# Performance work log

Hardware: AMD Instinct MI355X
Metric: run time of the kernel (lower is better)

## Reference

```python
import jax, jax.numpy as jnp
from jax import lax
import numpy as np

WS = 8      # window_size
SS = 4      # shift_size
NH = 8      # num_heads
DIM = 192
HID = int(DIM * 2.66)  # 510


def _rel_pos_index(ws):
    coords = np.stack(np.meshgrid(np.arange(ws), np.arange(ws), indexing='ij'))
    flat = coords.reshape(2, -1)
    rel = (flat[:, :, None] - flat[:, None, :]).transpose(1, 2, 0)
    rel[..., 0] += ws - 1
    rel[..., 1] += ws - 1
    rel[..., 0] *= 2 * ws - 1
    return rel.sum(-1)  # (ws*ws, ws*ws) int


def _attn_mask(Hp, Wp, ws, ss):
    img = np.zeros((Hp, Wp), dtype=np.float32)
    slices = (slice(0, -ws), slice(-ws, -ss), slice(-ss, None))
    cnt = 0
    for h in slices:
        for w in slices:
            img[h, w] = cnt
            cnt += 1
    mw = img.reshape(Hp // ws, ws, Wp // ws, ws).transpose(0, 2, 1, 3).reshape(-1, ws * ws)
    am = mw[:, None, :] - mw[:, :, None]
    return np.where(am != 0, -100.0, 0.0).astype(np.float32)  # (nW, N, N)


def _ln(t, w, b):
    mu = t.mean(-1, keepdims=True)
    var = t.var(-1, keepdims=True)
    return (t - mu) / jnp.sqrt(var + 1e-5) * w + b


def setup_inputs() -> dict:
    key = jax.random.key(0)
    ks = jax.random.split(key, 12)
    s = 0.05
    return {
        'x': jax.random.normal(ks[0], (2, DIM, 256, 256), jnp.float32),
        'norm1_w': jnp.ones((DIM,), jnp.float32),
        'norm1_b': jnp.zeros((DIM,), jnp.float32),
        'qkv_w': jax.random.normal(ks[1], (3 * DIM, DIM), jnp.float32) * s,
        'rpb_table': jax.random.normal(ks[2], ((2 * WS - 1) * (2 * WS - 1), NH), jnp.float32) * 0.02,
        'proj_w': jax.random.normal(ks[3], (DIM, DIM), jnp.float32) * s,
        'proj_b': jnp.zeros((DIM,), jnp.float32),
        'norm2_w': jnp.ones((DIM,), jnp.float32),
        'norm2_b': jnp.zeros((DIM,), jnp.float32),
        'pin_w': jax.random.normal(ks[4], (2 * HID, DIM), jnp.float32) * s,
        'dw_w': jax.random.normal(ks[5], (2 * HID, 1, 3, 3), jnp.float32) * s,
        'pout_w': jax.random.normal(ks[6], (DIM, HID), jnp.float32) * s,
    }


def reference(x, norm1_w, norm1_b, qkv_w, rpb_table, proj_w, proj_b,
              norm2_w, norm2_b, pin_w, dw_w, pout_w):
    B, C, H, W = x.shape
    hd = C // NH
    scale = hd ** -0.5

    # ---- norm1 (channel-last layernorm) ----
    xc = jnp.transpose(x, (0, 2, 3, 1))  # BHWC
    xn = _ln(xc, norm1_w, norm1_b)

    # ---- pad to window multiple ----
    pad_b = (WS - H % WS) % WS
    pad_r = (WS - W % WS) % WS
    xn = jnp.pad(xn, ((0, 0), (0, pad_b), (0, pad_r), (0, 0)))
    Hp, Wp = H + pad_b, W + pad_r

    # ---- cyclic shift ----
    sx = jnp.roll(xn, (-SS, -SS), axis=(1, 2))

    # ---- window partition ----
    nH, nW = Hp // WS, Wp // WS
    N = WS * WS
    xw = sx.reshape(B, nH, WS, nW, WS, C).transpose(0, 1, 3, 2, 4, 5)
    xw = xw.reshape(B * nH * nW, N, C)

    # ---- window attention ----
    qkv = (xw @ qkv_w.T).reshape(-1, N, 3, NH, hd).transpose(2, 0, 3, 1, 4)
    q, k, v = qkv[0] * scale, qkv[1], qkv[2]  # (B_, NH, N, hd)
    attn = jnp.einsum('bhnd,bhmd->bhnm', q, k)

    idx = _rel_pos_index(WS)
    bias = rpb_table[idx.reshape(-1)].reshape(N, N, NH).transpose(2, 0, 1)
    attn = attn + bias[None]

    mask = jnp.asarray(_attn_mask(Hp, Wp, WS, SS))  # (nWtot, N, N)
    nWtot = nH * nW
    attn = attn.reshape(B, nWtot, NH, N, N) + mask[None, :, None]
    attn = jax.nn.softmax(attn.reshape(-1, NH, N, N), axis=-1)

    out = jnp.einsum('bhnm,bhmd->bhnd', attn, v)
    out = out.transpose(0, 2, 1, 3).reshape(-1, N, C)
    out = out @ proj_w.T + proj_b

    # ---- window reverse + unshift + crop ----
    out = out.reshape(B, nH, nW, WS, WS, C).transpose(0, 1, 3, 2, 4, 5)
    out = out.reshape(B, Hp, Wp, C)
    out = jnp.roll(out, (SS, SS), axis=(1, 2))[:, :H, :W]
    x = x + jnp.transpose(out, (0, 3, 1, 2))

    # ---- FFN: 1x1 in -> depthwise 3x3 -> gated gelu -> 1x1 out ----
    y = _ln(jnp.transpose(x, (0, 2, 3, 1)), norm2_w, norm2_b)
    y = jnp.transpose(y, (0, 3, 1, 2))
    y = jnp.einsum('bchw,oc->bohw', y, pin_w)
    y = lax.conv_general_dilated(y, dw_w, (1, 1), 'SAME',
                                 feature_group_count=dw_w.shape[0],
                                 dimension_numbers=('NCHW', 'OIHW', 'NCHW'))
    h = dw_w.shape[0] // 2
    y = jax.nn.gelu(y[:, :h], approximate=False) * y[:, h:]
    y = jnp.einsum('bchw,oc->bohw', y, pout_w)
    return x + y
```

## Files before the change

### kernel.cpp

```cpp
#include <hip/hip_runtime.h>
#include <hip/hip_bf16.h>
#include <math.h>

#define CDIM 192
#define NTOK 131072
#define HD 24
#define NHEADS 8

typedef __attribute__((ext_vector_type(4))) float floatx4;
typedef __attribute__((ext_vector_type(8))) short bf16x8;

static __device__ __forceinline__ float bf2f(__hip_bfloat16 h) { return __bfloat162float(h); }
static __device__ __forceinline__ __hip_bfloat16 f2bf(float f) { return __float2bfloat16(f); }
static __device__ __forceinline__ float s2f(short s) {
  union { unsigned u; float f; } c; c.u = ((unsigned)(unsigned short)s) << 16; return c.f;
}
static __device__ __forceinline__ short f2s(float f) {
  __hip_bfloat16 h = __float2bfloat16(f);
  union { __hip_bfloat16 h; short s; } c; c.h = h; return c.s;
}
static __device__ __forceinline__ void load_lds16(const void* g, void* l) {
  __builtin_amdgcn_global_load_lds(
      (const __attribute__((address_space(1))) void*)g,
      (__attribute__((address_space(3))) void*)l, 16, 0, 0);
}

__global__ __launch_bounds__(256) void kcvt(
    const float* __restrict__ in, __hip_bfloat16* __restrict__ out, int n) {
  int i = blockIdx.x * 256 + threadIdx.x;
  if (i < n) out[i] = f2bf(in[i]);
}

__global__ __launch_bounds__(256) void k0_padpout(
    const float* __restrict__ w, __hip_bfloat16* __restrict__ o) {
  int idx = blockIdx.x * 256 + threadIdx.x;
  int n = idx >> 9, k = idx & 511;
  o[idx] = (k < 510) ? f2bf(w[n * 510 + k]) : f2bf(0.f);
}

__global__ __launch_bounds__(256) void k0_padpin(
    const float* __restrict__ w, __hip_bfloat16* __restrict__ o) {
  int idx = blockIdx.x * 256 + threadIdx.x;
  int n = idx / 192, k = idx % 192;
  int src = (n < 510) ? n : ((n >= 512 && n < 1022) ? n - 2 : -1);
  o[idx] = (src >= 0) ? f2bf(w[src * 192 + k]) : f2bf(0.f);
}

__global__ __launch_bounds__(256) void k0_wtap(
    const float* __restrict__ wdw, __hip_bfloat16* __restrict__ wa,
    __hip_bfloat16* __restrict__ wg) {
  int idx = blockIdx.x * 256 + threadIdx.x;
  if (idx >= 9 * 512) return;
  int tap = idx >> 9, c = idx & 511;
  wa[idx] = (c < 510) ? f2bf(wdw[c * 9 + tap]) : f2bf(0.f);
  wg[idx] = (c < 510) ? f2bf(wdw[(c + 510) * 9 + tap]) : f2bf(0.f);
}

__global__ __launch_bounds__(256) void k1_ln_raster(
    const float* __restrict__ x,
    const float* __restrict__ w,
    const float* __restrict__ bsh,
    __hip_bfloat16* __restrict__ out) {
  __shared__ float xs[32][193];
  int bid = blockIdx.x;
  int b = bid >> 11, si = (bid >> 3) & 255, sj0 = (bid & 7) << 5;
  int i = (si + 4) & 255;
  int tid = threadIdx.x;
  int lane = tid & 63, wv = tid >> 6;
  int p0 = (lane & 7) << 2;
  int cb = wv * 8 + (lane >> 3);
  int j4 = (sj0 + p0 + 4) & 255;
  long pbase = ((long)(b * CDIM + cb) << 16) + (i << 8) + j4;
  #pragma unroll
  for (int co = 0; co < 6; ++co) {
    floatx4 v = *(const floatx4*)(x + pbase + ((long)co << 21));
    int c = co * 32 + cb;
    xs[p0 + 0][c] = v[0];
    xs[p0 + 1][c] = v[1];
    xs[p0 + 2][c] = v[2];
    xs[p0 + 3][c] = v[3];
  }
  __syncthreads();
  int c0 = lane * 3;
  float w0 = w[c0], w1 = w[c0 + 1], w2 = w[c0 + 2];
  float g0 = bsh[c0], g1 = bsh[c0 + 1], g2 = bsh[c0 + 2];
  long tok0 = ((long)b << 16) + (si << 8) + sj0;
  for (int it = 0; it < 8; ++it) {
    int p = (wv << 3) + it;
    float v0 = xs[p][c0], v1 = xs[p][c0 + 1], v2 = xs[p][c0 + 2];
    float s = v0 + v1 + v2;
    float sq = v0 * v0 + v1 * v1 + v2 * v2;
    for (int off = 32; off; off >>= 1) { s += __shfl_xor(s, off); sq += __shfl_xor(sq, off); }
    float mean = s * (1.0f / 192.0f);
    float var  = sq * (1.0f / 192.0f) - mean * mean;
    float rstd = rsqrtf(var + 1e-5f);
    long tb = (tok0 + p) * CDIM + c0;
    out[tb    ] = f2bf((v0 - mean) * rstd * w0 + g0);
    out[tb + 1] = f2bf((v1 - mean) * rstd * w1 + g1);
    out[tb + 2] = f2bf((v2 - mean) * rstd * w2 + g2);
  }
}

template <int WM, int WN, int EPI>
__global__ __launch_bounds__(256) void gemm_lds(
    const __hip_bfloat16* __restrict__ A,
    const __hip_bfloat16* __restrict__ B,
    const float* __restrict__ bias,
    __hip_bfloat16* __restrict__ C,
    int K, int lda, int ldb, int ldc) {
  constexpr int BM = 32 * WM, BN = 32 * WN;
  __shared__ __hip_bfloat16 As[BM * 32];
  __shared__ __hip_bfloat16 Bs[BN * 32];
  int t = threadIdx.x;
  int wave = t >> 6, lane = t & 63;
  int wm = wave >> 1, wn = wave & 1;
  int r16 = lane & 15, quad = lane >> 4;
  long m0 = (long)blockIdx.y * BM;
  long n0 = (long)blockIdx.x * BN;
  int srow = t >> 2, scol = (t & 3) << 3;
  floatx4 acc[WM][WN];
  for (int i = 0; i < WM; ++i)
    for (int j = 0; j < WN; ++j)
      acc[i][j] = (floatx4){0.f, 0.f, 0.f, 0.f};
  for (int k0 = 0; k0 < K; k0 += 32) {
    __syncthreads();
    for (int p = 0; p < WM / 2; ++p)
      load_lds16(A + (m0 + srow + p * 64) * lda + k0 + scol,
                 (char*)As + t * 16 + p * 4096);
    for (int p = 0; p < WN / 2; ++p)
      load_lds16(B + (n0 + srow + p * 64) * ldb + k0 + scol,
                 (char*)Bs + t * 16 + p * 4096);
    __syncthreads();
    bf16x8 af[WM], bf[WN];
    for (int i = 0; i < WM; ++i)
      af[i] = *(const bf16x8*)&As[(wm * 16 * WM + i * 16 + r16) * 32 + quad * 8];
    for (int j = 0; j < WN; ++j)
      bf[j] = *(const bf16x8*)&Bs[(wn * 16 * WN + j * 16 + r16) * 32 + quad * 8];
    for (int i = 0; i < WM; ++i)
      for (int j = 0; j < WN; ++j)
        acc[i][j] = __builtin_amdgcn_mfma_f32_16x16x32_bf16(af[i], bf[j], acc[i][j], 0, 0, 0);
  }
  for (int i = 0; i < WM; ++i)
    for (int j = 0; j < WN; ++j) {
      int col = n0 + wn * 16 * WN + j * 16 + r16;
      float badd = (EPI == 1) ? bias[col] : 0.f;
      for (int r = 0; r < 4; ++r) {
        long row = m0 + wm * 16 * WM + i * 16 + quad * 4 + r;
        C[row * ldc + col] = f2bf(acc[i][j][r] + badd);
      }
    }
}

__global__ __launch_bounds__(256) void gemm_pout(
    const __hip_bfloat16* __restrict__ A,
    const __hip_bfloat16* __restrict__ B,
    const __hip_bfloat16* __restrict__ x2,
    float* __restrict__ out,
    int b, int r0) {
  constexpr int WM = 2, WN = 4, BM = 64, BN = 128;
  __shared__ __hip_bfloat16 As[BM * 32];
  __shared__ __hip_bfloat16 Bs[BN * 32];
  int t = threadIdx.x;
  int wave = t >> 6, lane = t & 63;
  int wm = wave >> 1, wn = wave & 1;
  int r16 = lane & 15, quad = lane >> 4;
  long m0 = (long)blockIdx.y * BM;
  long n0 = (long)blockIdx.x * BN;
  int srow = t >> 2, scol = (t & 3) << 3;
  floatx4 acc[WM][WN];
  for (int i = 0; i < WM; ++i)
    for (int j = 0; j < WN; ++j)
      acc[i][j] = (floatx4){0.f, 0.f, 0.f, 0.f};
  for (int k0 = 0; k0 < 512; k0 += 32) {
    __syncthreads();
    load_lds16(A + (m0 + srow) * 512 + k0 + scol, (char*)As + t * 16);
    for (int p = 0; p < WN / 2; ++p)
      load_lds16(B + (n0 + srow + p * 64) * 512 + k0 + scol,
                 (char*)Bs + t * 16 + p * 4096);
    __syncthreads();
    bf16x8 af[WM], bf[WN];
    for (int i = 0; i < WM; ++i)
      af[i] = *(const bf16x8*)&As[(wm * 16 * WM + i * 16 + r16) * 32 + quad * 8];
    for (int j = 0; j < WN; ++j)
      bf[j] = *(const bf16x8*)&Bs[(wn * 16 * WN + j * 16 + r16) * 32 + quad * 8];
    for (int i = 0; i < WM; ++i)
      for (int j = 0; j < WN; ++j)
        acc[i][j] = __builtin_amdgcn_mfma_f32_16x16x32_bf16(af[i], bf[j], acc[i][j], 0, 0, 0);
  }
  for (int i = 0; i < WM; ++i)
    for (int j = 0; j < WN; ++j) {
      int p_ = n0 + wn * 16 * WN + j * 16 + r16;
      int il = p_ >> 8, jj = p_ & 255;
      long pix = ((long)(r0 + il) << 8) + jj;
      for (int r = 0; r < 4; ++r) {
        int c_ = m0 + wm * 16 * WM + i * 16 + quad * 4 + r;
        long tok = ((long)b << 16) + pix;
        float v = acc[i][j][r] + bf2f(x2[tok * CDIM + c_]);
        out[((long)(b * CDIM + c_) << 16) + pix] = v;
      }
    }
}

__global__ __launch_bounds__(256) void k3_attn(
    const __hip_bfloat16* __restrict__ qkv,
    const float* __restrict__ rpb,
    __hip_bfloat16* __restrict__ out,
    int wid0) {
  __shared__ alignas(16) short Kp[64 * 32];
  __shared__ alignas(16) short Vt[32 * 64];
  __shared__ alignas(16) short Ps[4][16 * 64];
  __shared__ float rpbs[225];
  int h = blockIdx.x, widl = blockIdx.y;
  int wid = wid0 + widl;
  int t = threadIdx.x;
  int wv = t >> 6, lane = t & 63, quad = lane >> 4, r16 = lane & 15;
  int wi_l = widl >> 5, wjl = widl & 31;
  const short* qk = (const short*)qkv;

  if (t < 225) rpbs[t] = rpb[t * NHEADS + h];

  {
    int kr = t >> 2, kq = t & 3;
    bf16x8 kv = {0, 0, 0, 0, 0, 0, 0, 0};
    if (kq < 3) {
      long ltok = (long)((((wi_l << 3) + (kr >> 3)) << 8) + (wjl << 3) + (kr & 7));
      kv = *(const bf16x8*)(qk + ltok * 576 + 192 + h * HD + kq * 8);
    }
    *(bf16x8*)&Kp[kr * 32 + ((kq ^ ((kr >> 1) & 3)) << 3)] = kv;
  }
  {
    int tok = t & 63, q8 = t >> 6;
    if (q8 < 3) {
      long ltok = (long)((((wi_l << 3) + (tok >> 3)) << 8) + (wjl << 3) + (tok & 7));
      bf16x8 vv = *(const bf16x8*)(qk + ltok * 576 + 384 + h * HD + q8 * 8);
      #pragma unroll
      for (int e = 0; e < 8; ++e) {
        int d = q8 * 8 + e;
        Vt[d * 64 + (((tok >> 3) ^ (d & 7)) << 3) + (tok & 7)] = vv[e];
      }
    } else {
      int zt = t - 192;
      int d = 24 + (zt >> 3), tokg = zt & 7;
      bf16x8 z = {0, 0, 0, 0, 0, 0, 0, 0};
      *(bf16x8*)&Vt[d * 64 + ((tokg ^ (d & 7)) << 3)] = z;
    }
  }
  bf16x8 qf;
  {
    int nn = wv * 16 + r16;
    long ltok = (long)((((wi_l << 3) + (nn >> 3)) << 8) + (wjl << 3) + (nn & 7));
    qf = *(const bf16x8*)(qk + ltok * 576 + h * HD + quad * 8);
  }
  __syncthreads();

  floatx4 sj[4];
  int kswz = (quad ^ ((r16 >> 1) & 3)) << 3;
  #pragma unroll
  for (int j = 0; j < 4; ++j) {
    bf16x8 kf = *(const bf16x8*)&Kp[(j * 16 + r16) * 32 + kswz];
    sj[j] = __builtin_amdgcn_mfma_f32_16x16x32_bf16(
        qf, kf, (floatx4){0.f, 0.f, 0.f, 0.f}, 0, 0, 0);
  }

  int b = wid >> 10, wi = (wid >> 5) & 31, wj = wid & 31;
  int rkj[4];
  #pragma unroll
  for (int j = 0; j < 4; ++j) {
    int m = j * 16 + r16;
    int gsi = wi * 8 + (m >> 3), gsj = wj * 8 + (m & 7);
    rkj[j] = ((gsi < 248) ? 0 : (gsi < 252 ? 1 : 2)) * 3 +
             ((gsj < 248) ? 0 : (gsj < 252 ? 1 : 2));
  }

  float rs[4];
  #pragma unroll
  for (int r = 0; r < 4; ++r) {
    int n = wv * 16 + quad * 4 + r;
    int ti = n >> 3, tj = n & 7;
    int gi = wi * 8 + ti, gj = wj * 8 + tj;
    int rq = ((gi < 248) ? 0 : (gi < 252 ? 1 : 2)) * 3 +
             ((gj < 248) ? 0 : (gj < 252 ? 1 : 2));
    float val[4];
    float mx = -1e30f;
    #pragma unroll
    for (int j = 0; j < 4; ++j) {
      int m = j * 16 + r16;
      int idx = (ti - (m >> 3) + 7) * 15 + (tj - (m & 7) + 7);
      float v = sj[j][r] * 0.20412414523193154f + rpbs[idx];
      if (rkj[j] != rq) v -= 100.0f;
      val[j] = v;
      mx = fmaxf(mx, v);
    }
    #pragma unroll
    for (int off = 1; off < 16; off <<= 1) mx = fmaxf(mx, __shfl_xor(mx, off));
    float sum = 0.f;
    int row = quad * 4 + r;
    #pragma unroll
    for (int j = 0; j < 4; ++j) {
      float p = expf(val[j] - mx);
      sum += p;
      int col = j * 16 + r16;
      Ps[wv][row * 64 + ((((col >> 3) ^ (row & 7)) << 3)) + (col & 7)] = f2s(p);
    }
    #pragma unroll
    for (int off = 1; off < 16; off <<= 1) sum += __shfl_xor(sum, off);
    rs[r] = 1.0f / sum;
  }
  __syncthreads();

  floatx4 o0 = {0.f, 0.f, 0.f, 0.f}, o1 = {0.f, 0.f, 0.f, 0.f};
  #pragma unroll
  for (int kk = 0; kk < 2; ++kk) {
    int g = (((kk * 4 + quad) ^ (r16 & 7)) << 3);
    bf16x8 pa = *(const bf16x8*)&Ps[wv][r16 * 64 + g];
    bf16x8 b0 = *(const bf16x8*)&Vt[r16 * 64 + g];
    bf16x8 b1 = *(const bf16x8*)&Vt[(16 + r16) * 64 + g];
    o0 = __builtin_amdgcn_mfma_f32_16x16x32_bf16(pa, b0, o0, 0, 0, 0);
    o1 = __builtin_amdgcn_mfma_f32_16x16x32_bf16(pa, b1, o1, 0, 0, 0);
  }
  #pragma unroll
  for (int r = 0; r < 4; ++r) {
    int n = wv * 16 + quad * 4 + r;
    int gi = wi * 8 + (n >> 3), gj = wj * 8 + (n & 7);
    long ob = (((long)b << 16) + (gi << 8) + gj) * CDIM + h * HD;
    out[ob + r16] = f2bf(o0[r] * rs[r]);
    if (r16 < 8) out[ob + 16 + r16] = f2bf(o1[r] * rs[r]);
  }
}

__global__ __launch_bounds__(256) void k4_res_raster(
    const float* __restrict__ x,
    const __hip_bfloat16* __restrict__ tmp,
    __hip_bfloat16* __restrict__ x2,
    float* __restrict__ stats) {
  __shared__ float xs[32][193];
  int bid = blockIdx.x;
  int b = bid >> 11, i = (bid >> 3) & 255, j0 = (bid & 7) << 5;
  int tid = threadIdx.x;
  int lane = tid & 63, wv = tid >> 6;
  int p0 = (lane & 7) << 2;
  int cb = wv * 8 + (lane >> 3);
  long pbase = ((long)(b * CDIM + cb) << 16) + (i << 8) + j0 + p0;
  #pragma unroll
  for (int co = 0; co < 6; ++co) {
    floatx4 v = *(const floatx4*)(x + pbase + ((long)co << 21));
    int c = co * 32 + cb;
    xs[p0 + 0][c] = v[0];
    xs[p0 + 1][c] = v[1];
    xs[p0 + 2][c] = v[2];
    xs[p0 + 3][c] = v[3];
  }
  __syncthreads();
  int c0 = lane * 3;
  int si = (i + 252) & 255;
  for (int it = 0; it < 8; ++it) {
    int p = (wv << 3) + it;
    int j = j0 + p;
    int sj = (j + 252) & 255;
    long tsh = ((long)b << 16) + (si << 8) + sj;
    long sb = tsh * CDIM + c0;
    float v0 = xs[p][c0    ] + bf2f(tmp[sb    ]);
    float v1 = xs[p][c0 + 1] + bf2f(tmp[sb + 1]);
    float v2 = xs[p][c0 + 2] + bf2f(tmp[sb + 2]);
    long t2 = ((long)b << 16) + (i << 8) + j;
    long ob = t2 * CDIM + c0;
    x2[ob] = f2bf(v0); x2[ob + 1] = f2bf(v1); x2[ob + 2] = f2bf(v2);
    float s = v0 + v1 + v2, sq = v0 * v0 + v1 * v1 + v2 * v2;
    for (int off = 32; off; off >>= 1) { s += __shfl_xor(s, off); sq += __shfl_xor(sq, off); }
    float mean = s * (1.0f / 192.0f);
    float var  = sq * (1.0f / 192.0f) - mean * mean;
    float rstd = rsqrtf(var + 1e-5f);
    if (lane == 0) { stats[2 * t2] = mean; stats[2 * t2 + 1] = rstd; }
  }
}

__global__ __launch_bounds__(256) void k5_ln2(
    const __hip_bfloat16* __restrict__ x2,
    const float* __restrict__ stats,
    const float* __restrict__ nw,
    const float* __restrict__ nb,
    __hip_bfloat16* __restrict__ out,
    int b, int r0) {
  int idx = blockIdx.x * 256 + threadIdx.x;
  int tok = idx / 24, c0 = (idx % 24) << 3;
  int il = tok >> 8, j = tok & 255;
  int gi = r0 - 1 + il; gi = gi < 0 ? 0 : (gi > 255 ? 255 : gi);
  long t = ((long)b << 16) + (gi << 8) + j;
  float mean = stats[2 * t], rstd = stats[2 * t + 1];
  bf16x8 v = *(const bf16x8*)((const short*)x2 + t * CDIM + c0);
  bf16x8 r;
  for (int e = 0; e < 8; ++e)
    r[e] = f2s((s2f(v[e]) - mean) * rstd * nw[c0 + e] + nb[c0 + e]);
  *(bf16x8*)((short*)out + (long)tok * CDIM + c0) = r;
}

__global__ __launch_bounds__(256) void k7_dwgate(
    const __hip_bfloat16* __restrict__ pin,
    const __hip_bfloat16* __restrict__ wa,
    const __hip_bfloat16* __restrict__ wg,
    __hip_bfloat16* __restrict__ out,
    int r0) {
  int t = threadIdx.x;
  int oct = t & 63, pl = t >> 6;
  int p = blockIdx.x * 4 + pl;
  int il = p >> 8, j = p & 255;
  int gi = r0 + il;
  int c0 = oct << 3;
  float a[8], g[8];
  for (int e = 0; e < 8; ++e) { a[e] = 0.f; g[e] = 0.f; }
  for (int di = -1; di <= 1; ++di) {
    int ii = gi + di; if (ii < 0 || ii > 255) continue;
    int br = il + di + 1;
    for (int dj = -1; dj <= 1; ++dj) {
      int jj = j + dj; if (jj < 0 || jj > 255) continue;
      long nbase = ((long)((br << 8) + jj)) << 10;
      int tap = (di + 1) * 3 + (dj + 1);
      bf16x8 va  = *(const bf16x8*)((const short*)pin + nbase + c0);
      bf16x8 vg  = *(const bf16x8*)((const short*)pin + nbase + 512 + c0);
      bf16x8 wa8 = *(const bf16x8*)((const short*)wa + tap * 512 + c0);
      bf16x8 wg8 = *(const bf16x8*)((const short*)wg + tap * 512 + c0);
      for (int e = 0; e < 8; ++e) {
        a[e] += s2f(wa8[e]) * s2f(va[e]);
        g[e] += s2f(wg8[e]) * s2f(vg[e]);
      }
    }
  }
  bf16x8 r;
  for (int e = 0; e < 8; ++e) {
    float ge = 0.5f * a[e] * (1.0f + erff(a[e] * 0.70710678118654752f));
    r[e] = f2s(ge * g[e]);
  }
  *(bf16x8*)((short*)out + (long)p * 512 + c0) = r;
}

extern "C" void kernel_launch(void* const* d_in, const int* in_sizes, int n_in,
                              void* d_out, int out_size, void* d_ws, size_t ws_size,
                              hipStream_t stream) {
  const float* x       = (const float*)d_in[0];
  const float* norm1_w = (const float*)d_in[1];
  const float* norm1_b = (const float*)d_in[2];
  const float* qkv_w   = (const float*)d_in[3];
  const float* rpb     = (const float*)d_in[4];
  const float* proj_w  = (const float*)d_in[5];
  const float* proj_b  = (const float*)d_in[6];
  const float* norm2_w = (const float*)d_in[7];
  const float* norm2_b = (const float*)d_in[8];
  const float* pin_w   = (const float*)d_in[9];
  const float* dw_w    = (const float*)d_in[10];
  const float* pout_w  = (const float*)d_in[11];

  char* ws = (char*)d_ws;
  __hip_bfloat16* wsLN1 = (__hip_bfloat16*)(ws);
  __hip_bfloat16* wsPRJ = (__hip_bfloat16*)(ws);
  __hip_bfloat16* wsPINC= (__hip_bfloat16*)(ws);
  __hip_bfloat16* wsLN2C= (__hip_bfloat16*)(ws + 34603008UL);
  __hip_bfloat16* wsATT = (__hip_bfloat16*)(ws + 50331648UL);
  __hip_bfloat16* wsX2  = (__hip_bfloat16*)(ws + 50331648UL);
  float*          wsST  = (float*)         (ws + 100663296UL);
  __hip_bfloat16* wsGT  = (__hip_bfloat16*)(ws + 101711872UL);
  __hip_bfloat16* wsWA  = (__hip_bfloat16*)(ws + 118489088UL);
  __hip_bfloat16* wsWG  = (__hip_bfloat16*)(ws + 118507520UL);
  __hip_bfloat16* wsPW  = (__hip_bfloat16*)(ws + 120586240UL);
  __hip_bfloat16* wsQW  = (__hip_bfloat16*)(ws + 120782848UL);
  __hip_bfloat16* wsPJW = (__hip_bfloat16*)(ws + 121004032UL);
  __hip_bfloat16* wsPIW = (__hip_bfloat16*)(ws + 121077760UL);
  float* out = (float*)d_out;
  __hip_bfloat16* qkvbuf = (__hip_bfloat16*)d_out;

  kcvt<<<(110592 + 255) / 256, 256, 0, stream>>>(qkv_w, wsQW, 110592);
  kcvt<<<(36864 + 255) / 256, 256, 0, stream>>>(proj_w, wsPJW, 36864);
  k0_padpout<<<384, 256, 0, stream>>>(pout_w, wsPW);
  k0_padpin<<<768, 256, 0, stream>>>(pin_w, wsPIW);
  k1_ln_raster<<<4096, 256, 0, stream>>>(x, norm1_w, norm1_b, wsLN1);
  for (int b = 0; b < 2; ++b) {
    gemm_lds<4, 2, 0><<<dim3(9, 512), 256, 0, stream>>>(
        wsLN1 + (long)b * 65536 * CDIM, wsQW, nullptr, qkvbuf, 192, 192, 192, 576);
    k3_attn<<<dim3(8, 1024), 256, 0, stream>>>(qkvbuf, rpb, wsATT, b * 1024);
  }
  gemm_lds<4, 2, 1><<<dim3(3, 1024), 256, 0, stream>>>(
      wsATT, wsPJW, proj_b, wsPRJ, 192, 192, 192, 192);
  k4_res_raster<<<4096, 256, 0, stream>>>(x, wsPRJ, wsX2, wsST);
  k0_wtap<<<18, 256, 0, stream>>>(dw_w, wsWA, wsWG);
  for (int cc = 0; cc < 8; ++cc) {
    int b = cc >> 2, r0 = (cc & 3) * 64;
    k5_ln2<<<1584, 256, 0, stream>>>(wsX2, wsST, norm2_w, norm2_b, wsLN2C, b, r0);
    gemm_lds<4, 4, 0><<<dim3(8, 132), 256, 0, stream>>>(
        wsLN2C, wsPIW, nullptr, wsPINC, 192, 192, 192, 1024);
    k7_dwgate<<<4096, 256, 0, stream>>>(wsPINC, wsWA, wsWG, wsGT, r0);
    gemm_pout<<<dim3(128, 3), 256, 0, stream>>>(wsPW, wsGT, wsX2, out, b, r0);
  }
}
```

Before: 957.3 us.

## Fold LN2 into pin GEMM, head-major QKV layout, LDS-staged coalesced stores

Removes the separate LN2 kernel by folding norm2 weight into the pin weights and applying mean/rstd correction with precomputed per-column sums in the pin GEMM epilogue. The QKV GEMM now writes a head-major, per-head contiguous layout so attention loads K/V/Q as contiguous 24-element rows. The LN1 and residual kernels stage bf16 outputs in shared memory and write 16-byte coalesced stores instead of scalar stores. Attention uses fast __expf. The LN fold computes the normalization as a correction on raw-input bf16 products, which may lose precision.

After: 925.3 us. 3.3% less time.

```diff
diff --git a/kernel.cpp b/kernel.cpp
--- a/kernel.cpp
+++ b/kernel.cpp
@@ -6,6 +6,7 @@
 #define NTOK 131072
 #define HD 24
 #define NHEADS 8
+#define NTC 65536
 
 typedef __attribute__((ext_vector_type(4))) float floatx4;
 typedef __attribute__((ext_vector_type(8))) short bf16x8;
@@ -39,11 +40,26 @@
 }
 
 __global__ __launch_bounds__(256) void k0_padpin(
-    const float* __restrict__ w, __hip_bfloat16* __restrict__ o) {
+    const float* __restrict__ w, const float* __restrict__ nw,
+    __hip_bfloat16* __restrict__ o) {
   int idx = blockIdx.x * 256 + threadIdx.x;
   int n = idx / 192, k = idx % 192;
   int src = (n < 510) ? n : ((n >= 512 && n < 1022) ? n - 2 : -1);
-  o[idx] = (src >= 0) ? f2bf(w[src * 192 + k]) : f2bf(0.f);
+  o[idx] = (src >= 0) ? f2bf(w[src * 192 + k] * nw[k]) : f2bf(0.f);
+}
+
+__global__ __launch_bounds__(256) void k0_st(
+    const float* __restrict__ w, const float* __restrict__ nw,
+    const float* __restrict__ nb, float* __restrict__ S, float* __restrict__ T) {
+  int n = blockIdx.x * 256 + threadIdx.x;
+  int src = (n < 510) ? n : ((n >= 512 && n < 1022) ? n - 2 : -1);
+  float s = 0.f, t = 0.f;
+  if (src >= 0)
+    for (int c = 0; c < 192; ++c) {
+      float v = w[src * 192 + c];
+      s += v * nw[c]; t += v * nb[c];
+    }
+  S[n] = s; T[n] = t;
 }
 
 __global__ __launch_bounds__(256) void k0_wtap(
@@ -94,10 +110,19 @@
     float mean = s * (1.0f / 192.0f);
     float var  = sq * (1.0f / 192.0f) - mean * mean;
     float rstd = rsqrtf(var + 1e-5f);
-    long tb = (tok0 + p) * CDIM + c0;
-    out[tb    ] = f2bf((v0 - mean) * rstd * w0 + g0);
-    out[tb + 1] = f2bf((v1 - mean) * rstd * w1 + g1);
-    out[tb + 2] = f2bf((v2 - mean) * rstd * w2 + g2);
+    short* rowp = (short*)&xs[p][0];
+    rowp[c0    ] = f2s((v0 - mean) * rstd * w0 + g0);
+    rowp[c0 + 1] = f2s((v1 - mean) * rstd * w1 + g1);
+    rowp[c0 + 2] = f2s((v2 - mean) * rstd * w2 + g2);
+  }
+  __syncthreads();
+  char* gout = (char*)out + tok0 * 384;
+  #pragma unroll
+  for (int k = 0; k < 3; ++k) {
+    int o = k * 4096 + tid * 16;
+    int pt = o / 384, iw = (o % 384) >> 2;
+    floatx4 v = {xs[pt][iw], xs[pt][iw + 1], xs[pt][iw + 2], xs[pt][iw + 3]};
+    *(floatx4*)(gout + o) = v;
   }
 }
 
@@ -151,6 +176,120 @@
     }
 }
 
+__global__ __launch_bounds__(256) void gemm_qkv(
+    const __hip_bfloat16* __restrict__ A,
+    const __hip_bfloat16* __restrict__ B,
+    __hip_bfloat16* __restrict__ C) {
+  constexpr int WM = 4, WN = 2, BM = 128, BN = 64;
+  __shared__ __hip_bfloat16 As[BM * 32];
+  __shared__ __hip_bfloat16 Bs[BN * 32];
+  int t = threadIdx.x;
+  int wave = t >> 6, lane = t & 63;
+  int wm = wave >> 1, wn = wave & 1;
+  int r16 = lane & 15, quad = lane >> 4;
+  long m0 = (long)blockIdx.y * BM;
+  int n0 = blockIdx.x * BN;
+  int srow = t >> 2, scol = (t & 3) << 3;
+  floatx4 acc[WM][WN];
+  for (int i = 0; i < WM; ++i)
+    for (int j = 0; j < WN; ++j)
+      acc[i][j] = (floatx4){0.f, 0.f, 0.f, 0.f};
+  for (int k0 = 0; k0 < 192; k0 += 32) {
+    __syncthreads();
+    for (int p = 0; p < 2; ++p)
+      load_lds16(A + (m0 + srow + p * 64) * 192 + k0 + scol,
+                 (char*)As + t * 16 + p * 4096);
+    load_lds16(B + (n0 + srow) * 192 + k0 + scol, (char*)Bs + t * 16);
+    __syncthreads();
+    bf16x8 af[WM], bf[WN];
+    for (int i = 0; i < WM; ++i)
+      af[i] = *(const bf16x8*)&As[(wm * 64 + i * 16 + r16) * 32 + quad * 8];
+    for (int j = 0; j < WN; ++j)
+      bf[j] = *(const bf16x8*)&Bs[(wn * 32 + j * 16 + r16) * 32 + quad * 8];
+    for (int i = 0; i < WM; ++i)
+      for (int j = 0; j < WN; ++j)
+        acc[i][j] = __builtin_amdgcn_mfma_f32_16x16x32_bf16(af[i], bf[j], acc[i][j], 0, 0, 0);
+  }
+  for (int i = 0; i < WM; ++i)
+    for (int j = 0; j < WN; ++j) {
+      int col = n0 + wn * 32 + j * 16 + r16;
+      int sel = col / 192;
+      int cm = col - sel * 192;
+      int h = (cm * 683) >> 14;
+      int d = cm - h * 24;
+      long cb = (long)sel * (NTC * 192) + (long)h * (NTC * 24) + d;
+      for (int r = 0; r < 4; ++r) {
+        long row = m0 + wm * 64 + i * 16 + quad * 4 + r;
+        C[cb + row * 24] = f2bf(acc[i][j][r]);
+      }
+    }
+}
+
+__global__ __launch_bounds__(256) void gemm_pin(
+    const __hip_bfloat16* __restrict__ x2,
+    const __hip_bfloat16* __restrict__ B,
+    const float* __restrict__ stats,
+    const float* __restrict__ Sv,
+    const float* __restrict__ Tv,
+    __hip_bfloat16* __restrict__ C,
+    int bb, int r0) {
+  constexpr int WM = 4, WN = 4, BM = 128, BN = 128;
+  __shared__ __hip_bfloat16 As[BM * 32];
+  __shared__ __hip_bfloat16 Bs[BN * 32];
+  int t = threadIdx.x;
+  int wave = t >> 6, lane = t & 63;
+  int wm = wave >> 1, wn = wave & 1;
+  int r16 = lane & 15, quad = lane >> 4;
+  int m0 = blockIdx.y * BM;
+  int n0 = blockIdx.x * BN;
+  int srow = t >> 2, scol = (t & 3) << 3;
+  floatx4 acc[WM][WN];
+  for (int i = 0; i < WM; ++i)
+    for (int j = 0; j < WN; ++j)
+      acc[i][j] = (floatx4){0.f, 0.f, 0.f, 0.f};
+  for (int k0 = 0; k0 < 192; k0 += 32) {
+    __syncthreads();
+    for (int p = 0; p < 2; ++p) {
+      int rr = m0 + srow + p * 64;
+      int il = rr >> 8, jj = rr & 255;
+      int gi = r0 - 1 + il; gi = gi < 0 ? 0 : (gi > 255 ? 255 : gi);
+      long tok = ((long)bb << 16) + (gi << 8) + jj;
+      load_lds16(x2 + tok * 192 + k0 + scol, (char*)As + t * 16 + p * 4096);
+    }
+    for (int p = 0; p < 2; ++p)
+      load_lds16(B + (n0 + srow + p * 64) * 192 + k0 + scol,
+                 (char*)Bs + t * 16 + p * 4096);
+    __syncthreads();
+    bf16x8 af[WM], bf[WN];
+    for (int i = 0; i < WM; ++i)
+      af[i] = *(const bf16x8*)&As[(wm * 64 + i * 16 + r16) * 32 + quad * 8];
+    for (int j = 0; j < WN; ++j)
+      bf[j] = *(const bf16x8*)&Bs[(wn * 64 + j * 16 + r16) * 32 + quad * 8];
+    for (int i = 0; i < WM; ++i)
+      for (int j = 0; j < WN; ++j)
+        acc[i][j] = __builtin_amdgcn_mfma_f32_16x16x32_bf16(af[i], bf[j], acc[i][j], 0, 0, 0);
+  }
+  for (int i = 0; i < WM; ++i) {
+    float mr[4], rsd[4];
+    #pragma unroll
+    for (int r = 0; r < 4; ++r) {
+      int row = m0 + wm * 64 + i * 16 + quad * 4 + r;
+      int il = row >> 8, jj = row & 255;
+      int gi = r0 - 1 + il; gi = gi < 0 ? 0 : (gi > 255 ? 255 : gi);
+      long tok = ((long)bb << 16) + (gi << 8) + jj;
+      mr[r] = stats[2 * tok]; rsd[r] = stats[2 * tok + 1];
+    }
+    for (int j = 0; j < WN; ++j) {
+      int col = n0 + wn * 64 + j * 16 + r16;
+      float sv = Sv[col], tv = Tv[col];
+      for (int r = 0; r < 4; ++r) {
+        int row = m0 + wm * 64 + i * 16 + quad * 4 + r;
+        C[(long)row * 1024 + col] = f2bf(acc[i][j][r] * rsd[r] - mr[r] * rsd[r] * sv + tv);
+      }
+    }
+  }
+}
+
 __global__ __launch_bounds__(256) void gemm_pout(
     const __hip_bfloat16* __restrict__ A,
     const __hip_bfloat16* __restrict__ B,
@@ -216,6 +355,9 @@
   int wv = t >> 6, lane = t & 63, quad = lane >> 4, r16 = lane & 15;
   int wi_l = widl >> 5, wjl = widl & 31;
   const short* qk = (const short*)qkv;
+  const short* Qp  = qk + (long)h * (NTC * 24);
+  const short* Kpg = Qp + (long)NTC * 192;
+  const short* Vpg = Qp + (long)NTC * 384;
 
   if (t < 225) rpbs[t] = rpb[t * NHEADS + h];
 
@@ -223,16 +365,16 @@
     int kr = t >> 2, kq = t & 3;
     bf16x8 kv = {0, 0, 0, 0, 0, 0, 0, 0};
     if (kq < 3) {
-      long ltok = (long)((((wi_l << 3) + (kr >> 3)) << 8) + (wjl << 3) + (kr & 7));
-      kv = *(const bf16x8*)(qk + ltok * 576 + 192 + h * HD + kq * 8);
+      int ltok = ((((wi_l << 3) + (kr >> 3)) << 8) + (wjl << 3) + (kr & 7));
+      kv = *(const bf16x8*)(Kpg + (long)ltok * 24 + kq * 8);
     }
     *(bf16x8*)&Kp[kr * 32 + ((kq ^ ((kr >> 1) & 3)) << 3)] = kv;
   }
   {
     int tok = t & 63, q8 = t >> 6;
     if (q8 < 3) {
-      long ltok = (long)((((wi_l << 3) + (tok >> 3)) << 8) + (wjl << 3) + (tok & 7));
-      bf16x8 vv = *(const bf16x8*)(qk + ltok * 576 + 384 + h * HD + q8 * 8);
+      int ltok = ((((wi_l << 3) + (tok >> 3)) << 8) + (wjl << 3) + (tok & 7));
+      bf16x8 vv = *(const bf16x8*)(Vpg + (long)ltok * 24 + q8 * 8);
       #pragma unroll
       for (int e = 0; e < 8; ++e) {
         int d = q8 * 8 + e;
@@ -248,8 +390,8 @@
   bf16x8 qf;
   {
     int nn = wv * 16 + r16;
-    long ltok = (long)((((wi_l << 3) + (nn >> 3)) << 8) + (wjl << 3) + (nn & 7));
-    qf = *(const bf16x8*)(qk + ltok * 576 + h * HD + quad * 8);
+    int ltok = ((((wi_l << 3) + (nn >> 3)) << 8) + (wjl << 3) + (nn & 7));
+    qf = *(const bf16x8*)(Qp + (long)ltok * 24 + quad * 8);
   }
   __syncthreads();
 
@@ -297,7 +439,7 @@
     int row = quad * 4 + r;
     #pragma unroll
     for (int j = 0; j < 4; ++j) {
-      float p = expf(val[j] - mx);
+      float p = __expf(val[j] - mx);
       sum += p;
       int col = j * 16 + r16;
       Ps[wv][row * 64 + ((((col >> 3) ^ (row & 7)) << 3)) + (col & 7)] = f2s(p);
@@ -362,36 +504,30 @@
     float v0 = xs[p][c0    ] + bf2f(tmp[sb    ]);
     float v1 = xs[p][c0 + 1] + bf2f(tmp[sb + 1]);
     float v2 = xs[p][c0 + 2] + bf2f(tmp[sb + 2]);
-    long t2 = ((long)b << 16) + (i << 8) + j;
-    long ob = t2 * CDIM + c0;
-    x2[ob] = f2bf(v0); x2[ob + 1] = f2bf(v1); x2[ob + 2] = f2bf(v2);
     float s = v0 + v1 + v2, sq = v0 * v0 + v1 * v1 + v2 * v2;
     for (int off = 32; off; off >>= 1) { s += __shfl_xor(s, off); sq += __shfl_xor(sq, off); }
     float mean = s * (1.0f / 192.0f);
     float var  = sq * (1.0f / 192.0f) - mean * mean;
     float rstd = rsqrtf(var + 1e-5f);
-    if (lane == 0) { stats[2 * t2] = mean; stats[2 * t2 + 1] = rstd; }
-  }
-}
-
-__global__ __launch_bounds__(256) void k5_ln2(
-    const __hip_bfloat16* __restrict__ x2,
-    const float* __restrict__ stats,
-    const float* __restrict__ nw,
-    const float* __restrict__ nb,
-    __hip_bfloat16* __restrict__ out,
-    int b, int r0) {
-  int idx = blockIdx.x * 256 + threadIdx.x;
-  int tok = idx / 24, c0 = (idx % 24) << 3;
-  int il = tok >> 8, j = tok & 255;
-  int gi = r0 - 1 + il; gi = gi < 0 ? 0 : (gi > 255 ? 255 : gi);
-  long t = ((long)b << 16) + (gi << 8) + j;
-  float mean = stats[2 * t], rstd = stats[2 * t + 1];
-  bf16x8 v = *(const bf16x8*)((const short*)x2 + t * CDIM + c0);
-  bf16x8 r;
-  for (int e = 0; e < 8; ++e)
-    r[e] = f2s((s2f(v[e]) - mean) * rstd * nw[c0 + e] + nb[c0 + e]);
-  *(bf16x8*)((short*)out + (long)tok * CDIM + c0) = r;
+    short* rowp = (short*)&xs[p][0];
+    rowp[c0    ] = f2s(v0);
+    rowp[c0 + 1] = f2s(v1);
+    rowp[c0 + 2] = f2s(v2);
+    if (lane == 0) {
+      long t2 = ((long)b << 16) + (i << 8) + j;
+      stats[2 * t2] = mean; stats[2 * t2 + 1] = rstd;
+    }
+  }
+  __syncthreads();
+  long t20 = ((long)b << 16) + (i << 8) + j0;
+  char* gout = (char*)x2 + t20 * 384;
+  #pragma unroll
+  for (int k = 0; k < 3; ++k) {
+    int o = k * 4096 + tid * 16;
+    int pt = o / 384, iw = (o % 384) >> 2;
+    floatx4 v = {xs[pt][iw], xs[pt][iw + 1], xs[pt][iw + 2], xs[pt][iw + 3]};
+    *(floatx4*)(gout + o) = v;
+  }
 }
 
 __global__ __launch_bounds__(256) void k7_dwgate(
@@ -453,13 +589,14 @@
   __hip_bfloat16* wsLN1 = (__hip_bfloat16*)(ws);
   __hip_bfloat16* wsPRJ = (__hip_bfloat16*)(ws);
   __hip_bfloat16* wsPINC= (__hip_bfloat16*)(ws);
-  __hip_bfloat16* wsLN2C= (__hip_bfloat16*)(ws + 34603008UL);
   __hip_bfloat16* wsATT = (__hip_bfloat16*)(ws + 50331648UL);
   __hip_bfloat16* wsX2  = (__hip_bfloat16*)(ws + 50331648UL);
   float*          wsST  = (float*)         (ws + 100663296UL);
   __hip_bfloat16* wsGT  = (__hip_bfloat16*)(ws + 101711872UL);
   __hip_bfloat16* wsWA  = (__hip_bfloat16*)(ws + 118489088UL);
   __hip_bfloat16* wsWG  = (__hip_bfloat16*)(ws + 118507520UL);
+  float*          wsS   = (float*)         (ws + 118517760UL);
+  float*          wsT   = (float*)         (ws + 118525952UL);
   __hip_bfloat16* wsPW  = (__hip_bfloat16*)(ws + 120586240UL);
   __hip_bfloat16* wsQW  = (__hip_bfloat16*)(ws + 120782848UL);
   __hip_bfloat16* wsPJW = (__hip_bfloat16*)(ws + 121004032UL);
@@ -470,22 +607,22 @@
   kcvt<<<(110592 + 255) / 256, 256, 0, stream>>>(qkv_w, wsQW, 110592);
   kcvt<<<(36864 + 255) / 256, 256, 0, stream>>>(proj_w, wsPJW, 36864);
   k0_padpout<<<384, 256, 0, stream>>>(pout_w, wsPW);
-  k0_padpin<<<768, 256, 0, stream>>>(pin_w, wsPIW);
+  k0_padpin<<<768, 256, 0, stream>>>(pin_w, norm2_w, wsPIW);
+  k0_st<<<4, 256, 0, stream>>>(pin_w, norm2_w, norm2_b, wsS, wsT);
+  k0_wtap<<<18, 256, 0, stream>>>(dw_w, wsWA, wsWG);
   k1_ln_raster<<<4096, 256, 0, stream>>>(x, norm1_w, norm1_b, wsLN1);
   for (int b = 0; b < 2; ++b) {
-    gemm_lds<4, 2, 0><<<dim3(9, 512), 256, 0, stream>>>(
-        wsLN1 + (long)b * 65536 * CDIM, wsQW, nullptr, qkvbuf, 192, 192, 192, 576);
+    gemm_qkv<<<dim3(9, 512), 256, 0, stream>>>(
+        wsLN1 + (long)b * 65536 * CDIM, wsQW, qkvbuf);
     k3_attn<<<dim3(8, 1024), 256, 0, stream>>>(qkvbuf, rpb, wsATT, b * 1024);
   }
   gemm_lds<4, 2, 1><<<dim3(3, 1024), 256, 0, stream>>>(
       wsATT, wsPJW, proj_b, wsPRJ, 192, 192, 192, 192);
   k4_res_raster<<<4096, 256, 0, stream>>>(x, wsPRJ, wsX2, wsST);
-  k0_wtap<<<18, 256, 0, stream>>>(dw_w, wsWA, wsWG);
   for (int cc = 0; cc < 8; ++cc) {
     int b = cc >> 2, r0 = (cc & 3) * 64;
-    k5_ln2<<<1584, 256, 0, stream>>>(wsX2, wsST, norm2_w, norm2_b, wsLN2C, b, r0);
-    gemm_lds<4, 4, 0><<<dim3(8, 132), 256, 0, stream>>>(
-        wsLN2C, wsPIW, nullptr, wsPINC, 192, 192, 192, 1024);
+    gemm_pin<<<dim3(8, 132), 256, 0, stream>>>(
+        wsX2, wsPIW, wsST, wsS, wsT, wsPINC, b, r0);
     k7_dwgate<<<4096, 256, 0, stream>>>(wsPINC, wsWA, wsWG, wsGT, r0);
     gemm_pout<<<dim3(128, 3), 256, 0, stream>>>(wsPW, wsGT, wsX2, out, b, r0);
   }
```
